# Kernel optimization log

Measured on AMD Instinct MI355X. Metric: run time of the kernel, lower is better.

Reference implementation:

```python
import jax, jax.numpy as jnp
import numpy as np

ALPHA = 1.5
BETA = 45.0
LAMDA = 0.5
B = 8192   # batch_size
D = 128    # feature dim (hardcoded in original via zeros((1,128)))
V = 4      # number of views stacked in fj
EPS = 1e-12  # F.normalize eps


def _l2norm_rows(x):
    n = jnp.sqrt(jnp.sum(x * x, axis=-1, keepdims=True))
    return x / jnp.maximum(n, EPS)


def setup_inputs() -> dict:
    key = jax.random.key(0)
    k1, k2 = jax.random.split(key)
    fi = jax.random.normal(k1, (B, D), dtype=jnp.float32)
    fj = jax.random.normal(k2, (V, B, D), dtype=jnp.float32)
    # L2-normalize embeddings so exp(beta*(SVM - lamda)) stays finite (beta=45)
    fi = _l2norm_rows(fi)
    fj = _l2norm_rows(fj)
    return {"fi": fi, "fj": fj, "b": V}


def avg_svm(fi, fj):
    # Original: per-row softmax-weighted average of fj rows, renormalized,
    # dotted with fi row, averaged over the batch.
    A = fi @ fj.T                      # [B, B] pairwise logits
    W = jax.nn.softmax(A, axis=1)      # softmax over j (alphalist / sumofalpha)
    Vw = W @ fj                        # [B, D] softmax-weighted averages
    Vn = _l2norm_rows(Vw)              # F.normalize(p=2, dim=1)
    return jnp.mean(jnp.sum(fi * Vn, axis=1))  # mean_i fi[i] . Vn[i]


def reference(fi, fj, b):
    b = int(b)
    # SMM1 is recomputed identically every outer iteration in the original;
    # compute once and multiply the per-iteration term by (b-1).
    smm1 = avg_svm(fi, fi)
    if b > 2:
        # inner loop: SMM2sum is a running (cumulative) sum over j=1..b-2,
        # and exp(beta*(SMM2sum - lamda)) is added at every step.
        s_vals = jnp.stack([avg_svm(fi, fj[j]) for j in range(1, b - 1)])
        cum = jnp.cumsum(s_vals)
        ssum = jnp.sum(jnp.exp(BETA * (cum - LAMDA)))
    else:
        ssum = jnp.exp(BETA * (avg_svm(fi, fj) - LAMDA))
    term = (1.0 / ALPHA) * jnp.log1p(jnp.exp(-ALPHA * (smm1 - LAMDA))) \
         + (1.0 / BETA) * jnp.log1p(ssum)
    loss = (b - 1) * term
    return jnp.squeeze(loss)
```

## Files before the change

kernel.cpp:

```cpp
#include <hip/hip_runtime.h>

#define BDIM 8192
#define DDIM 128

typedef __attribute__((ext_vector_type(4))) float floatx4;
typedef __attribute__((ext_vector_type(4))) int   intx4;
typedef __attribute__((ext_vector_type(8))) int   intx8;
typedef long i64;

#define SLAB (BDIM * DDIM)
#define G8_OFF 64
#define G8T_OFF (64 + 3 * SLAB)

__device__ inline void load_lds16(const void* g, void* l) {
    __builtin_amdgcn_global_load_lds(
        (const __attribute__((address_space(1))) unsigned int*)g,
        (__attribute__((address_space(3))) unsigned int*)l, 16, 0, 0);
}

__device__ inline intx8 ld_pair(const char* base, int c0) {
    union { intx8 v; intx4 h[2]; } u;
    u.h[0] = *(const intx4*)(base + c0 * 16);
    u.h[1] = *(const intx4*)(base + (c0 ^ 1) * 16);
    return u.v;
}

__device__ inline float exp_fast(float x) {
    return __builtin_amdgcn_exp2f(x * 1.44269504088896341f);
}

__global__ __launch_bounds__(256)
void prep_kernel(const float* __restrict__ fi, const float* __restrict__ fj,
                 unsigned char* __restrict__ g8, unsigned char* __restrict__ g8T,
                 float* __restrict__ acc)
{
    const int p = blockIdx.y;
    const int kblock = blockIdx.x;
    const int rbase = kblock * 32;
    const int tid = threadIdx.x;
    if (p == 0 && kblock == 0 && tid < 8) acc[tid] = 0.f;
    const float* src = (p == 0) ? fi : (fj + (size_t)p * SLAB);

    __shared__ __align__(16) unsigned char T8[32][144];

    {
        const int row = tid >> 3, c = tid & 7;
        const float* sp = src + (size_t)(rbase + row) * DDIM + c * 16;
        float4 f0 = ((const float4*)sp)[0];
        float4 f1 = ((const float4*)sp)[1];
        float4 f2 = ((const float4*)sp)[2];
        float4 f3 = ((const float4*)sp)[3];
        alignas(16) int w[4];
        w[0] = __builtin_amdgcn_cvt_pk_fp8_f32(f0.x, f0.y, 0, false);
        w[0] = __builtin_amdgcn_cvt_pk_fp8_f32(f0.z, f0.w, w[0], true);
        w[1] = __builtin_amdgcn_cvt_pk_fp8_f32(f1.x, f1.y, 0, false);
        w[1] = __builtin_amdgcn_cvt_pk_fp8_f32(f1.z, f1.w, w[1], true);
        w[2] = __builtin_amdgcn_cvt_pk_fp8_f32(f2.x, f2.y, 0, false);
        w[2] = __builtin_amdgcn_cvt_pk_fp8_f32(f2.z, f2.w, w[2], true);
        w[3] = __builtin_amdgcn_cvt_pk_fp8_f32(f3.x, f3.y, 0, false);
        w[3] = __builtin_amdgcn_cvt_pk_fp8_f32(f3.z, f3.w, w[3], true);
        int4 v = *(int4*)w;
        *(int4*)(g8 + (size_t)p * SLAB + (size_t)(rbase + row) * DDIM + c * 16) = v;
        *(int4*)(&T8[row][c * 16]) = v;
    }
    __syncthreads();
    {
        const int d = tid >> 1, half = tid & 1;
        const int s = (d >> 2) & 3;
        alignas(16) unsigned char bb[16];
        #pragma unroll
        for (int x = 0; x < 16; ++x) {
            int g  = (half << 1) + (x >> 3);
            int u  = x & 7;
            int kl = ((g ^ s) << 2) + (u & 3) + ((u >> 2) << 4);
            bb[x] = T8[kl][d];
        }
        *(int4*)(g8T + (size_t)p * SLAB + (size_t)kblock * 4096 + d * 32 + half * 16) =
            *(int4*)bb;
    }
}

__global__ __launch_bounds__(256, 3)
void flash_kernel(const float* __restrict__ fi,
                  const unsigned char* __restrict__ g8,
                  const unsigned char* __restrict__ g8T,
                  float* __restrict__ acc)
{
    const int b = blockIdx.x;
    const int gp = (b & 7) * 96 + (b >> 3);
    const int p = gp >> 8;
    const int qbase = (gp & 255) * 32;
    const int tid = threadIdx.x;
    const int wave = tid >> 6, lane = tid & 63;
    const int quad = lane >> 4, col = lane & 15;

    __shared__ __align__(16) char smem[17408];
    #define KOFF 0
    #define OOFF 0
    #define PVOFF 16896

    const unsigned char* g8p  = g8  + (size_t)p * SLAB;
    const unsigned char* g8Tp = g8T + (size_t)p * SLAB;

    intx8 qf[2];
    #pragma unroll
    for (int qt = 0; qt < 2; ++qt) {
        const intx4* qp = (const intx4*)(g8 + (size_t)(qbase + qt * 16 + col) * DDIM +
                                         quad * 32);
        union { intx8 v; intx4 h[2]; } u;
        u.h[0] = qp[0];
        u.h[1] = qp[1];
        qf[qt] = u.v;
    }

    floatx4 O[2][8];
    #pragma unroll
    for (int qt = 0; qt < 2; ++qt)
        #pragma unroll
        for (int dt = 0; dt < 8; ++dt)
            O[qt][dt] = (floatx4){0.f, 0.f, 0.f, 0.f};

    const unsigned char* kSrc = g8p + (size_t)wave * 4096 +
        (size_t)(lane >> 3) * 128 + (size_t)(((lane & 7) ^ ((lane >> 3) & 7)) * 16);

    auto stageK = [&]() {
        #pragma unroll
        for (int i = 0; i < 4; ++i)
            load_lds16(kSrc + i * 1024, smem + KOFF + wave * 4096 + i * 1024);
        kSrc += 16384;
    };

    const char* kb0 = smem + KOFF + wave * 4096 + col * 128;
    const char* kb1 = smem + KOFF + wave * 4096 + (16 + col) * 128;
    const int   kc  = (quad * 2) ^ (col & 7);

    const unsigned char* gVb = g8Tp + (size_t)wave * 4096 +
                               (size_t)col * 32 + (size_t)((quad ^ (col >> 2)) * 8);

    stageK();

    for (int k = 0; k < 64; ++k) {
        asm volatile("s_waitcnt vmcnt(0)" ::: "memory");

        i64 vf[8];
        #pragma unroll
        for (int dt = 0; dt < 8; ++dt)
            vf[dt] = *(const i64*)(gVb + dt * 512);
        gVb += 16384;

        intx8 kf0 = ld_pair(kb0, kc);
        intx8 kf1 = ld_pair(kb1, kc);
        asm volatile("s_waitcnt lgkmcnt(0)" ::: "memory");
        stageK();

        floatx4 S[2][2];
        __builtin_amdgcn_s_setprio(1);
        S[0][0] = __builtin_amdgcn_mfma_scale_f32_16x16x128_f8f6f4(
            kf0, qf[0], (floatx4){0.f,0.f,0.f,0.f}, 0, 0, 0, 127, 0, 127);
        S[0][1] = __builtin_amdgcn_mfma_scale_f32_16x16x128_f8f6f4(
            kf0, qf[1], (floatx4){0.f,0.f,0.f,0.f}, 0, 0, 0, 127, 0, 127);
        S[1][0] = __builtin_amdgcn_mfma_scale_f32_16x16x128_f8f6f4(
            kf1, qf[0], (floatx4){0.f,0.f,0.f,0.f}, 0, 0, 0, 127, 0, 127);
        S[1][1] = __builtin_amdgcn_mfma_scale_f32_16x16x128_f8f6f4(
            kf1, qf[1], (floatx4){0.f,0.f,0.f,0.f}, 0, 0, 0, 127, 0, 127);
        __builtin_amdgcn_s_setprio(0);

        i64 pf[2];
        #pragma unroll
        for (int qt = 0; qt < 2; ++qt) {
            int w0 = __builtin_amdgcn_cvt_pk_fp8_f32(
                exp_fast(S[0][qt][0]), exp_fast(S[0][qt][1]), 0, false);
            w0 = __builtin_amdgcn_cvt_pk_fp8_f32(
                exp_fast(S[0][qt][2]), exp_fast(S[0][qt][3]), w0, true);
            int w1 = __builtin_amdgcn_cvt_pk_fp8_f32(
                exp_fast(S[1][qt][0]), exp_fast(S[1][qt][1]), 0, false);
            w1 = __builtin_amdgcn_cvt_pk_fp8_f32(
                exp_fast(S[1][qt][2]), exp_fast(S[1][qt][3]), w1, true);
            union { i64 l; int i[2]; } u;
            u.i[0] = w0;
            u.i[1] = w1;
            pf[qt] = u.l;
        }

        asm volatile("s_waitcnt vmcnt(4)" ::: "memory");

        __builtin_amdgcn_s_setprio(1);
        #pragma unroll
        for (int qt = 0; qt < 2; ++qt)
            #pragma unroll
            for (int dt = 0; dt < 8; ++dt)
                O[qt][dt] = __builtin_amdgcn_mfma_f32_16x16x32_fp8_fp8(
                    pf[qt], vf[dt], O[qt][dt], 0, 0, 0);
        __builtin_amdgcn_s_setprio(0);
    }

    asm volatile("s_waitcnt vmcnt(0)" ::: "memory");
    __syncthreads();

    float* OL = (float*)(smem + OOFF);
    #pragma unroll 1
    for (int w = 0; w < 4; ++w) {
        if (wave == w) {
            #pragma unroll
            for (int qt = 0; qt < 2; ++qt)
                #pragma unroll
                for (int dt = 0; dt < 8; ++dt)
                    #pragma unroll
                    for (int r = 0; r < 4; ++r) {
                        const int q = qt * 16 + quad * 4 + r;
                        const int d = dt * 16 + col;
                        if (w == 0) OL[q * 132 + d]  = O[qt][dt][r];
                        else        OL[q * 132 + d] += O[qt][dt][r];
                    }
        }
        __syncthreads();
    }

    {
        const int q = tid >> 3, dc = (tid & 7) * 16;
        const float* fq = fi + (size_t)(qbase + q) * DDIM + dc;
        float dot = 0.f, nr = 0.f;
        #pragma unroll
        for (int u = 0; u < 16; ++u) {
            float o = OL[q * 132 + dc + u];
            dot += fq[u] * o;
            nr  += o * o;
        }
        #pragma unroll
        for (int m = 1; m < 8; m <<= 1) {
            dot += __shfl_xor(dot, m, 64);
            nr  += __shfl_xor(nr,  m, 64);
        }
        float* pv = (float*)(smem + PVOFF);
        if ((tid & 7) == 0)
            pv[q] = dot * rsqrtf(fmaxf(nr, 1e-30f));
        __syncthreads();
        if (tid < 32) {
            float val = pv[tid];
            #pragma unroll
            for (int m = 1; m < 32; m <<= 1) val += __shfl_xor(val, m, 64);
            if (tid == 0) atomicAdd(&acc[p], val);
        }
    }
}

__global__ void final_kernel(const float* __restrict__ acc, float* __restrict__ out)
{
    if (threadIdx.x == 0 && blockIdx.x == 0) {
        const double s0 = (double)acc[0] / (double)BDIM;
        const double s1 = (double)acc[1] / (double)BDIM;
        const double s2 = (double)acc[2] / (double)BDIM;
        const double t1 = (1.0 / 1.5) * log1p(exp(-1.5 * (s0 - 0.5)));
        const double ssum = exp(45.0 * (s1 - 0.5)) + exp(45.0 * (s1 + s2 - 0.5));
        const double t2 = (1.0 / 45.0) * log1p(ssum);
        out[0] = (float)(3.0 * (t1 + t2));
    }
}

extern "C" void kernel_launch(void* const* d_in, const int* in_sizes, int n_in,
                              void* d_out, int out_size, void* d_ws, size_t ws_size,
                              hipStream_t stream)
{
    const float* fi = (const float*)d_in[0];
    const float* fj = (const float*)d_in[1];

    float* acc = (float*)d_ws;
    unsigned char* g8  = (unsigned char*)d_ws + G8_OFF;
    unsigned char* g8T = (unsigned char*)d_ws + G8T_OFF;

    prep_kernel <<<dim3(BDIM / 32, 3), 256, 0, stream>>>(fi, fj, g8, g8T, acc);
    flash_kernel<<<dim3(768), 256, 0, stream>>>(fi, g8, g8T, acc);
    final_kernel<<<1, 64, 0, stream>>>(acc, (float*)d_out);
}
```

Measured before the change: 170.4 us.

## Switch flash kernel to 32x32x64 MFMA tiles with LDS-staged V

```diff
diff --git a/kernel.cpp b/kernel.cpp
--- a/kernel.cpp
+++ b/kernel.cpp
@@ -3,9 +3,10 @@
 #define BDIM 8192
 #define DDIM 128
 
-typedef __attribute__((ext_vector_type(4))) float floatx4;
-typedef __attribute__((ext_vector_type(4))) int   intx4;
-typedef __attribute__((ext_vector_type(8))) int   intx8;
+typedef __attribute__((ext_vector_type(4)))  float floatx4;
+typedef __attribute__((ext_vector_type(16))) float floatx16;
+typedef __attribute__((ext_vector_type(4)))  int   intx4;
+typedef __attribute__((ext_vector_type(8)))  int   intx8;
 typedef long i64;
 
 #define SLAB (BDIM * DDIM)
@@ -65,18 +66,18 @@
     }
     __syncthreads();
     {
-        const int d = tid >> 1, half = tid & 1;
-        const int s = (d >> 2) & 3;
+        const int o  = kblock >> 3;
+        const int t  = (kblock >> 2) & 1;
+        const int wv = kblock & 3;
+        unsigned char* region = g8T + (size_t)p * SLAB +
+                                (size_t)o * 32768 + (size_t)wv * 8192;
+        const int d = tid >> 1, h = tid & 1;
+        const int pos = ((h << 1) + t) ^ ((d >> 1) & 3);
         alignas(16) unsigned char bb[16];
         #pragma unroll
-        for (int x = 0; x < 16; ++x) {
-            int g  = (half << 1) + (x >> 3);
-            int u  = x & 7;
-            int kl = ((g ^ s) << 2) + (u & 3) + ((u >> 2) << 4);
-            bb[x] = T8[kl][d];
-        }
-        *(int4*)(g8T + (size_t)p * SLAB + (size_t)kblock * 4096 + d * 32 + half * 16) =
-            *(int4*)bb;
+        for (int r = 0; r < 16; ++r)
+            bb[r] = T8[(r & 3) + 8 * (r >> 2) + 4 * h][d];
+        *(int4*)(region + d * 64 + pos * 16) = *(int4*)bb;
     }
 }
 
@@ -92,106 +93,119 @@
     const int qbase = (gp & 255) * 32;
     const int tid = threadIdx.x;
     const int wave = tid >> 6, lane = tid & 63;
-    const int quad = lane >> 4, col = lane & 15;
-
-    __shared__ __align__(16) char smem[17408];
+    const int col32 = lane & 31, h = lane >> 5;
+
+    __shared__ __align__(16) char smem[49152];
     #define KOFF 0
+    #define VOFF 16384
     #define OOFF 0
     #define PVOFF 16896
 
     const unsigned char* g8p  = g8  + (size_t)p * SLAB;
     const unsigned char* g8Tp = g8T + (size_t)p * SLAB;
 
-    intx8 qf[2];
+    const unsigned char* qrow = g8 + (size_t)(qbase + col32) * DDIM + h * 32;
+    intx8 qf0 = *(const intx8*)(qrow);
+    intx8 qf1 = *(const intx8*)(qrow + 64);
+
+    floatx16 Z16;
     #pragma unroll
-    for (int qt = 0; qt < 2; ++qt) {
-        const intx4* qp = (const intx4*)(g8 + (size_t)(qbase + qt * 16 + col) * DDIM +
-                                         quad * 32);
-        union { intx8 v; intx4 h[2]; } u;
-        u.h[0] = qp[0];
-        u.h[1] = qp[1];
-        qf[qt] = u.v;
-    }
-
-    floatx4 O[2][8];
-    #pragma unroll
-    for (int qt = 0; qt < 2; ++qt)
-        #pragma unroll
-        for (int dt = 0; dt < 8; ++dt)
-            O[qt][dt] = (floatx4){0.f, 0.f, 0.f, 0.f};
+    for (int i = 0; i < 16; ++i) Z16[i] = 0.f;
+    floatx16 O0 = Z16, O1 = Z16, O2 = Z16, O3 = Z16;
 
     const unsigned char* kSrc = g8p + (size_t)wave * 4096 +
         (size_t)(lane >> 3) * 128 + (size_t)(((lane & 7) ^ ((lane >> 3) & 7)) * 16);
-
     auto stageK = [&]() {
         #pragma unroll
         for (int i = 0; i < 4; ++i)
             load_lds16(kSrc + i * 1024, smem + KOFF + wave * 4096 + i * 1024);
         kSrc += 16384;
     };
-
-    const char* kb0 = smem + KOFF + wave * 4096 + col * 128;
-    const char* kb1 = smem + KOFF + wave * 4096 + (16 + col) * 128;
-    const int   kc  = (quad * 2) ^ (col & 7);
-
-    const unsigned char* gVb = g8Tp + (size_t)wave * 4096 +
-                               (size_t)col * 32 + (size_t)((quad ^ (col >> 2)) * 8);
+    const unsigned char* vSrc = g8Tp + (size_t)wave * 8192 + (size_t)lane * 16;
+    auto stageV = [&]() {
+        #pragma unroll
+        for (int i = 0; i < 8; ++i)
+            load_lds16(vSrc + i * 1024, smem + VOFF + wave * 8192 + i * 1024);
+        vSrc += 32768;
+    };
+
+    const char* kb  = smem + KOFF + wave * 4096 + col32 * 128;
+    const int   kcc = col32 & 7;
+    const char* vbw = smem + VOFF + wave * 8192 + col32 * 64;
+    const int   vs  = (2 * h) ^ ((col32 >> 1) & 3);
 
     stageK();
-
-    for (int k = 0; k < 64; ++k) {
+    stageV();
+
+    #pragma unroll 1
+    for (int o = 0; o < 32; ++o) {
+        intx8 pa;
+
+        asm volatile("s_waitcnt vmcnt(8)" ::: "memory");
+        {
+            intx8 kf0 = ld_pair(kb, (2 * h) ^ kcc);
+            intx8 kf1 = ld_pair(kb, (4 + 2 * h) ^ kcc);
+            asm volatile("s_waitcnt lgkmcnt(0)" ::: "memory");
+            stageK();
+            floatx16 S = Z16;
+            __builtin_amdgcn_s_setprio(1);
+            S = __builtin_amdgcn_mfma_scale_f32_32x32x64_f8f6f4(
+                kf0, qf0, S, 0, 0, 0, 127, 0, 127);
+            S = __builtin_amdgcn_mfma_scale_f32_32x32x64_f8f6f4(
+                kf1, qf1, S, 0, 0, 0, 127, 0, 127);
+            __builtin_amdgcn_s_setprio(0);
+            #pragma unroll
+            for (int j = 0; j < 4; ++j) {
+                int wv = __builtin_amdgcn_cvt_pk_fp8_f32(
+                    exp_fast(S[4 * j]), exp_fast(S[4 * j + 1]), 0, false);
+                wv = __builtin_amdgcn_cvt_pk_fp8_f32(
+                    exp_fast(S[4 * j + 2]), exp_fast(S[4 * j + 3]), wv, true);
+                pa[j] = wv;
+            }
+        }
+
         asm volatile("s_waitcnt vmcnt(0)" ::: "memory");
-
-        i64 vf[8];
-        #pragma unroll
-        for (int dt = 0; dt < 8; ++dt)
-            vf[dt] = *(const i64*)(gVb + dt * 512);
-        gVb += 16384;
-
-        intx8 kf0 = ld_pair(kb0, kc);
-        intx8 kf1 = ld_pair(kb1, kc);
-        asm volatile("s_waitcnt lgkmcnt(0)" ::: "memory");
-        stageK();
-
-        floatx4 S[2][2];
-        __builtin_amdgcn_s_setprio(1);
-        S[0][0] = __builtin_amdgcn_mfma_scale_f32_16x16x128_f8f6f4(
-            kf0, qf[0], (floatx4){0.f,0.f,0.f,0.f}, 0, 0, 0, 127, 0, 127);
-        S[0][1] = __builtin_amdgcn_mfma_scale_f32_16x16x128_f8f6f4(
-            kf0, qf[1], (floatx4){0.f,0.f,0.f,0.f}, 0, 0, 0, 127, 0, 127);
-        S[1][0] = __builtin_amdgcn_mfma_scale_f32_16x16x128_f8f6f4(
-            kf1, qf[0], (floatx4){0.f,0.f,0.f,0.f}, 0, 0, 0, 127, 0, 127);
-        S[1][1] = __builtin_amdgcn_mfma_scale_f32_16x16x128_f8f6f4(
-            kf1, qf[1], (floatx4){0.f,0.f,0.f,0.f}, 0, 0, 0, 127, 0, 127);
-        __builtin_amdgcn_s_setprio(0);
-
-        i64 pf[2];
-        #pragma unroll
-        for (int qt = 0; qt < 2; ++qt) {
-            int w0 = __builtin_amdgcn_cvt_pk_fp8_f32(
-                exp_fast(S[0][qt][0]), exp_fast(S[0][qt][1]), 0, false);
-            w0 = __builtin_amdgcn_cvt_pk_fp8_f32(
-                exp_fast(S[0][qt][2]), exp_fast(S[0][qt][3]), w0, true);
-            int w1 = __builtin_amdgcn_cvt_pk_fp8_f32(
-                exp_fast(S[1][qt][0]), exp_fast(S[1][qt][1]), 0, false);
-            w1 = __builtin_amdgcn_cvt_pk_fp8_f32(
-                exp_fast(S[1][qt][2]), exp_fast(S[1][qt][3]), w1, true);
-            union { i64 l; int i[2]; } u;
-            u.i[0] = w0;
-            u.i[1] = w1;
-            pf[qt] = u.l;
+        {
+            intx8 kf0 = ld_pair(kb, (2 * h) ^ kcc);
+            intx8 kf1 = ld_pair(kb, (4 + 2 * h) ^ kcc);
+            asm volatile("s_waitcnt lgkmcnt(0)" ::: "memory");
+            stageK();
+            floatx16 S = Z16;
+            __builtin_amdgcn_s_setprio(1);
+            S = __builtin_amdgcn_mfma_scale_f32_32x32x64_f8f6f4(
+                kf0, qf0, S, 0, 0, 0, 127, 0, 127);
+            S = __builtin_amdgcn_mfma_scale_f32_32x32x64_f8f6f4(
+                kf1, qf1, S, 0, 0, 0, 127, 0, 127);
+            __builtin_amdgcn_s_setprio(0);
+            #pragma unroll
+            for (int j = 0; j < 4; ++j) {
+                int wv = __builtin_amdgcn_cvt_pk_fp8_f32(
+                    exp_fast(S[4 * j]), exp_fast(S[4 * j + 1]), 0, false);
+                wv = __builtin_amdgcn_cvt_pk_fp8_f32(
+                    exp_fast(S[4 * j + 2]), exp_fast(S[4 * j + 3]), wv, true);
+                pa[4 + j] = wv;
+            }
         }
 
         asm volatile("s_waitcnt vmcnt(4)" ::: "memory");
-
-        __builtin_amdgcn_s_setprio(1);
-        #pragma unroll
-        for (int qt = 0; qt < 2; ++qt)
-            #pragma unroll
-            for (int dt = 0; dt < 8; ++dt)
-                O[qt][dt] = __builtin_amdgcn_mfma_f32_16x16x32_fp8_fp8(
-                    pf[qt], vf[dt], O[qt][dt], 0, 0, 0);
-        __builtin_amdgcn_s_setprio(0);
+        {
+            intx8 vf0 = ld_pair(vbw,        vs);
+            intx8 vf1 = ld_pair(vbw + 2048, vs);
+            intx8 vf2 = ld_pair(vbw + 4096, vs);
+            intx8 vf3 = ld_pair(vbw + 6144, vs);
+            asm volatile("s_waitcnt lgkmcnt(0)" ::: "memory");
+            if (o < 31) stageV();
+            __builtin_amdgcn_s_setprio(1);
+            O0 = __builtin_amdgcn_mfma_scale_f32_32x32x64_f8f6f4(
+                pa, vf0, O0, 0, 0, 0, 127, 0, 127);
+            O1 = __builtin_amdgcn_mfma_scale_f32_32x32x64_f8f6f4(
+                pa, vf1, O1, 0, 0, 0, 127, 0, 127);
+            O2 = __builtin_amdgcn_mfma_scale_f32_32x32x64_f8f6f4(
+                pa, vf2, O2, 0, 0, 0, 127, 0, 127);
+            O3 = __builtin_amdgcn_mfma_scale_f32_32x32x64_f8f6f4(
+                pa, vf3, O3, 0, 0, 0, 127, 0, 127);
+            __builtin_amdgcn_s_setprio(0);
+        }
     }
 
     asm volatile("s_waitcnt vmcnt(0)" ::: "memory");
@@ -202,16 +216,16 @@
     for (int w = 0; w < 4; ++w) {
         if (wave == w) {
             #pragma unroll
-            for (int qt = 0; qt < 2; ++qt)
+            for (int db = 0; db < 4; ++db)
                 #pragma unroll
-                for (int dt = 0; dt < 8; ++dt)
-                    #pragma unroll
-                    for (int r = 0; r < 4; ++r) {
-                        const int q = qt * 16 + quad * 4 + r;
-                        const int d = dt * 16 + col;
-                        if (w == 0) OL[q * 132 + d]  = O[qt][dt][r];
-                        else        OL[q * 132 + d] += O[qt][dt][r];
-                    }
+                for (int r = 0; r < 16; ++r) {
+                    const int q = (r & 3) + 8 * (r >> 2) + 4 * h;
+                    const int d = db * 32 + col32;
+                    const float v = (db == 0) ? O0[r] : (db == 1) ? O1[r]
+                                  : (db == 2) ? O2[r] : O3[r];
+                    if (w == 0) OL[q * 132 + d]  = v;
+                    else        OL[q * 132 + d] += v;
+                }
         }
         __syncthreads();
     }
@@ -222,9 +236,9 @@
         float dot = 0.f, nr = 0.f;
         #pragma unroll
         for (int u = 0; u < 16; ++u) {
-            float o = OL[q * 132 + dc + u];
-            dot += fq[u] * o;
-            nr  += o * o;
+            float ov = OL[q * 132 + dc + u];
+            dot += fq[u] * ov;
+            nr  += ov * ov;
         }
         #pragma unroll
         for (int m = 1; m < 8; m <<= 1) {
```

After: 202.6 us. +18.9%, slower.
